# Performance work log

Measured on AMD Instinct MI355X. Metric: run time of the kernel, lower is better.

## Reference

```python
import jax, jax.numpy as jnp
import numpy as np


def _conv(x, w, pad):
    # NCHW conv, stride 1
    return jax.lax.conv_general_dilated(
        x, w, (1, 1), [(pad, pad), (pad, pad)],
        dimension_numbers=('NCHW', 'OIHW', 'NCHW'))


def _bn_relu(x, s, b, m, v):
    # eval-mode BatchNorm2d (running stats) + ReLU, eps=1e-5
    inv = s / jnp.sqrt(v + 1e-5)
    return jax.nn.relu(x * inv[None, :, None, None] + (b - m * inv)[None, :, None, None])


def _pam(x, qw, qb, kw, kb, vw, vb, gamma):
    B, C, H, W = x.shape
    N = H * W
    q = (_conv(x, qw, 0) + qb[None, :, None, None]).reshape(B, -1, N)  # [B,Cr,N]
    k = (_conv(x, kw, 0) + kb[None, :, None, None]).reshape(B, -1, N)  # [B,Cr,N]
    v = (_conv(x, vw, 0) + vb[None, :, None, None]).reshape(B, C, N)   # [B,C,N]
    energy = jnp.einsum('bcn,bcm->bnm', q, k)          # [B,N,N], query n over keys m
    att = jax.nn.softmax(energy, axis=-1)
    out = jnp.einsum('bcm,bnm->bcn', v, att).reshape(B, C, H, W)
    return gamma * out + x


def _cam(x, gamma):
    B, C, H, W = x.shape
    f = x.reshape(B, C, -1)                            # [B,C,N]
    energy = jnp.einsum('bcn,bdn->bcd', f, f)          # [B,C,C]
    energy_new = jnp.max(energy, axis=-1, keepdims=True) - energy
    att = jax.nn.softmax(energy_new, axis=-1)
    out = jnp.einsum('bcd,bdn->bcn', att, f).reshape(B, C, H, W)
    return gamma * out + x


def _forward(x, w5a, bn5a_s, bn5a_b, bn5a_m, bn5a_v,
             pq_w, pq_b, pk_w, pk_b, pv_w, pv_b, p_gamma,
             w51, bn51_s, bn51_b, bn51_m, bn51_v,
             w5c, bn5c_s, bn5c_b, bn5c_m, bn5c_v, c_gamma,
             w52, bn52_s, bn52_b, bn52_m, bn52_v,
             w8, b8):
    feat1 = _bn_relu(_conv(x, w5a, 1), bn5a_s, bn5a_b, bn5a_m, bn5a_v)
    sa_feat = _pam(feat1, pq_w, pq_b, pk_w, pk_b, pv_w, pv_b, p_gamma)
    sa_conv = _bn_relu(_conv(sa_feat, w51, 1), bn51_s, bn51_b, bn51_m, bn51_v)
    feat2 = _bn_relu(_conv(x, w5c, 1), bn5c_s, bn5c_b, bn5c_m, bn5c_v)
    sc_feat = _cam(feat2, c_gamma)
    sc_conv = _bn_relu(_conv(sc_feat, w52, 1), bn52_s, bn52_b, bn52_m, bn52_v)
    feat_sum = sa_conv + sc_conv
    # conv8 = Dropout2d (identity in eval) -> 1x1 conv -> ReLU
    sasc = jax.nn.relu(_conv(feat_sum, w8, 0) + b8[None, :, None, None])
    return sasc


def setup_inputs() -> dict:
    key = jax.random.key(0)
    ks = iter(jax.random.split(key, 48))
    def rn(shape, scale=0.1):
        return jax.random.normal(next(ks), shape, jnp.float32) * scale
    def bn_params(c):
        s = rn((c,), 0.2) + 1.0
        b = rn((c,), 0.1)
        m = rn((c,), 0.1)
        v = jnp.abs(rn((c,), 0.5)) + 0.5
        return s, b, m, v
    Cin, Ci, Cout = 512, 32, 2
    Cr = max(1, Ci // 8)  # = 4
    inp = {}
    inp['x'] = jax.random.normal(next(ks), (4, Cin, 64, 64), jnp.float32)
    inp['w5a'] = rn((Ci, Cin, 3, 3), 0.05)
    inp['bn5a_s'], inp['bn5a_b'], inp['bn5a_m'], inp['bn5a_v'] = bn_params(Ci)
    inp['pq_w'] = rn((Cr, Ci, 1, 1)); inp['pq_b'] = rn((Cr,), 0.01)
    inp['pk_w'] = rn((Cr, Ci, 1, 1)); inp['pk_b'] = rn((Cr,), 0.01)
    inp['pv_w'] = rn((Ci, Ci, 1, 1)); inp['pv_b'] = rn((Ci,), 0.01)
    inp['p_gamma'] = jnp.full((1,), 0.5, jnp.float32)
    inp['w51'] = rn((Ci, Ci, 3, 3))
    inp['bn51_s'], inp['bn51_b'], inp['bn51_m'], inp['bn51_v'] = bn_params(Ci)
    inp['w5c'] = rn((Ci, Cin, 3, 3), 0.05)
    inp['bn5c_s'], inp['bn5c_b'], inp['bn5c_m'], inp['bn5c_v'] = bn_params(Ci)
    inp['c_gamma'] = jnp.full((1,), 0.5, jnp.float32)
    inp['w52'] = rn((Ci, Ci, 3, 3))
    inp['bn52_s'], inp['bn52_b'], inp['bn52_m'], inp['bn52_v'] = bn_params(Ci)
    inp['w8'] = rn((Cout, Ci, 1, 1)); inp['b8'] = rn((Cout,), 0.01)
    return inp


def reference(x, w5a, bn5a_s, bn5a_b, bn5a_m, bn5a_v,
              pq_w, pq_b, pk_w, pk_b, pv_w, pv_b, p_gamma,
              w51, bn51_s, bn51_b, bn51_m, bn51_v,
              w5c, bn5c_s, bn5c_b, bn5c_m, bn5c_v, c_gamma,
              w52, bn52_s, bn52_b, bn52_m, bn52_v,
              w8, b8):
    return _forward(x, w5a, bn5a_s, bn5a_b, bn5a_m, bn5a_v,
                    pq_w, pq_b, pk_w, pk_b, pv_w, pv_b, p_gamma,
                    w51, bn51_s, bn51_b, bn51_m, bn51_v,
                    w5c, bn5c_s, bn5c_b, bn5c_m, bn5c_v, c_gamma,
                    w52, bn52_s, bn52_b, bn52_m, bn52_v,
                    w8, b8)
```

## Files before the change

kernel.cpp:

```cpp
#include <hip/hip_runtime.h>
#include <hip/hip_bf16.h>


typedef __attribute__((ext_vector_type(8))) short bf16x8;
typedef __attribute__((ext_vector_type(4))) float f32x4;

#define O_WPK   0
#define O_W51P  147456
#define O_W52P  152064
#define O_BNA   156672
#define O_W8    156928
#define O_PQW   157000
#define O_PKW   157132
#define O_PVW   157264
#define O_GAM   158320
#define O_Q     158400
#define O_K     223936
#define O_ENE   453312
#define O_F1T   985792
#define O_F2T   1510080
#define O_V     2034368
#define O_SAT   2558656
#define O_SCT   2837440
#define O_XT    461504
#define O_CP    4922048
#define O_PO    4922048
#define O_PS    3116224
#define O_PE2   9437184

__device__ __forceinline__ unsigned short f2b(float f){
  __hip_bfloat16 h = __float2bfloat16(f);
  return *(unsigned short*)&h;
}

__global__ __launch_bounds__(256) void k_prep_nhwc(
  const float* __restrict__ x,
  const float* w5a, const float* w5c,
  const float* w51, const float* w52,
  const float* s0,const float* b0,const float* m0,const float* v0,
  const float* s1,const float* b1,const float* m1,const float* v1,
  const float* s2,const float* b2,const float* m2,const float* v2,
  const float* s3,const float* b3,const float* m3,const float* v3,
  const float* w8,const float* b8,
  const float* pqw,const float* pqb,const float* pkw,const float* pkb,
  const float* pvw,const float* pvb,const float* pg,const float* cg,
  float* ws)
{
  int bx = blockIdx.x;
  int tid = threadIdx.x;
  __shared__ unsigned short t16[64][65];
  if (bx < 2048){
    int y = bx & 63, ct = (bx >> 6) & 7, b = bx >> 9;
    int r0 = tid >> 4, c0 = (tid & 15) * 4;
    const float* xb = x + ((size_t)(b*512 + ct*64))*4096 + y*64;
    #pragma unroll
    for (int i = 0; i < 4; ++i){
      int row = r0 + i*16;
      float4 v = *(const float4*)(xb + (size_t)row*4096 + c0);
      t16[row][c0+0] = f2b(v.x);
      t16[row][c0+1] = f2b(v.y);
      t16[row][c0+2] = f2b(v.z);
      t16[row][c0+3] = f2b(v.w);
    }
    __syncthreads();
    int pixl = tid >> 2, q = tid & 3;
    unsigned short vs[16];
    #pragma unroll
    for (int j = 0; j < 16; ++j) vs[j] = t16[q*16 + j][pixl];
    unsigned u[8];
    #pragma unroll
    for (int j = 0; j < 8; ++j) u[j] = (unsigned)vs[2*j] | ((unsigned)vs[2*j+1] << 16);
    unsigned short* xt = (unsigned short*)(ws + O_XT);
    int cbl = ct*2 + (q>>1);
    size_t off = (((size_t)(b*16 + cbl)*66 + (y+1))*66 + (pixl+1))*32 + (q&1)*16;
    *(uint4*)(xt + off)     = make_uint4(u[0],u[1],u[2],u[3]);
    *(uint4*)(xt + off + 8) = make_uint4(u[4],u[5],u[6],u[7]);
    return;
  }
  int pbx = bx - 2048;
  if (pbx < 1152){
    int id = pbx*256 + tid;
    int tap = id >> 15;
    int r = id & 32767;
    int cb = r >> 11;
    int r2 = r & 2047;
    int co = r2 >> 5, ci = r2 & 31;
    int cin = cb*32 + ci;
    float v = (co < 32) ? w5a[co*4608 + cin*9 + tap] : w5c[(co-32)*4608 + cin*9 + tap];
    ((unsigned short*)ws)[id] = f2b(v);
    return;
  }
  if (pbx < 1231){
    int id = (pbx-1152)*256 + tid;
    if (id >= 20076) return;
    if (id < 9216){ int tap=id>>10, co=(id>>5)&31, ci=id&31;
      ((unsigned short*)(ws + O_W51P))[id] = f2b(w51[co*288 + ci*9 + tap]); return; }
    id -= 9216;
    if (id < 9216){ int tap=id>>10, co=(id>>5)&31, ci=id&31;
      ((unsigned short*)(ws + O_W52P))[id] = f2b(w52[co*288 + ci*9 + tap]); return; }
    id -= 9216;
    if (id < 256){
      int conv = id>>6, ab = (id>>5)&1, c = id&31;
      const float *S,*Bb,*M,*V;
      if (conv==0){S=s0;Bb=b0;M=m0;V=v0;} else if (conv==1){S=s1;Bb=b1;M=m1;V=v1;}
      else if (conv==2){S=s2;Bb=b2;M=m2;V=v2;} else {S=s3;Bb=b3;M=m3;V=v3;}
      float A = S[c] * rsqrtf(V[c] + 1e-5f);
      ws[O_BNA + conv*64 + ab*32 + c] = ab ? (Bb[c] - M[c]*A) : A;
      return; }
    id -= 256;
    if (id < 64){ ws[O_W8+id] = w8[id]; return; } id -= 64;
    if (id < 2){ ws[O_W8+64+id] = b8[id]; return; } id -= 2;
    if (id < 128){ ws[O_PQW+id] = pqw[id]; return; } id -= 128;
    if (id < 4){ ws[O_PQW+128+id] = pqb[id]; return; } id -= 4;
    if (id < 128){ ws[O_PKW+id] = pkw[id]; return; } id -= 128;
    if (id < 4){ ws[O_PKW+128+id] = pkb[id]; return; } id -= 4;
    if (id < 1024){ ws[O_PVW+id] = pvw[id]; return; } id -= 1024;
    if (id < 32){ ws[O_PVW+1024+id] = pvb[id]; return; } id -= 32;
    ws[O_GAM+id] = id ? cg[0] : pg[0];
    return;
  }
  {
    int i = (pbx-1231)*256 + tid;
    if (i >= 66560) return;
    int part = i & 3; int j = i >> 2;
    int rp = j % 260; int bc = j / 260;
    int py, px;
    if (rp < 66){ py = 0; px = rp; }
    else if (rp < 132){ py = 65; px = rp - 66; }
    else if (rp < 196){ py = rp - 131; px = 0; }
    else { py = rp - 195; px = 65; }
    size_t off = (((size_t)bc*66 + py)*66 + px)*32 + part*8;
    *(uint4*)((unsigned short*)(ws + O_XT) + off) = make_uint4(0,0,0,0);
  }
}

__global__ __launch_bounds__(256) void k_conv_mfma(float* __restrict__ ws){
  int mb = blockIdx.x;
  int ks = blockIdx.y;
  int b = mb >> 6, y = mb & 63;
  __shared__ unsigned short Bs[198*40];
  int tid = threadIdx.x;
  int w = tid >> 6, l = tid & 63;
  f32x4 zero = {0.f,0.f,0.f,0.f};
  f32x4 acc[4] = {zero, zero, zero, zero};
  const unsigned short* wp = (const unsigned short*)ws;
  const unsigned short* xt = (const unsigned short*)(ws + O_XT);
  int arow = w*16 + (l & 15);
  int kq = (l >> 4)*8;
  int i0 = tid, i1 = tid + 256, i2 = tid + 512, i3 = tid + 768;
  const unsigned short* slab0 = xt + ((size_t)((b*16 + ks*4)*66 + y))*2112;
  uint4 r0 = *(const uint4*)(slab0 + i0*8);
  uint4 r1 = *(const uint4*)(slab0 + i1*8);
  uint4 r2 = *(const uint4*)(slab0 + i2*8);
  uint4 r3 = (tid < 24) ? *(const uint4*)(slab0 + i3*8) : make_uint4(0,0,0,0);
  for (int cb4 = 0; cb4 < 4; ++cb4){
    int cb = ks*4 + cb4;
    __syncthreads();
    *(uint4*)&Bs[(i0>>2)*40 + (i0&3)*8] = r0;
    *(uint4*)&Bs[(i1>>2)*40 + (i1&3)*8] = r1;
    *(uint4*)&Bs[(i2>>2)*40 + (i2&3)*8] = r2;
    if (tid < 24) *(uint4*)&Bs[(i3>>2)*40 + (i3&3)*8] = r3;
    __syncthreads();
    if (cb4 < 3){
      const unsigned short* slab = xt + ((size_t)((b*16 + cb + 1)*66 + y))*2112;
      r0 = *(const uint4*)(slab + i0*8);
      r1 = *(const uint4*)(slab + i1*8);
      r2 = *(const uint4*)(slab + i2*8);
      if (tid < 24) r3 = *(const uint4*)(slab + i3*8);
    }
    #pragma unroll
    for (int tap = 0; tap < 9; ++tap){
      int dy = tap/3, dx = tap - dy*3;
      bf16x8 af = *(const bf16x8*)(wp + (size_t)(tap*16 + cb)*2048 + arow*32 + kq);
      #pragma unroll
      for (int pt = 0; pt < 4; ++pt){
        int pix = pt*16 + (l&15) + dx;
        bf16x8 bv = *(const bf16x8*)&Bs[(dy*66 + pix)*40 + kq];
        acc[pt] = __builtin_amdgcn_mfma_f32_16x16x32_bf16(af, bv, acc[pt], 0, 0, 0);
      }
    }
  }
  float* cp = ws + O_CP + ((size_t)(ks*4 + b))*262144;
  int co0 = w*16 + (l>>4)*4;
  #pragma unroll
  for (int pt = 0; pt < 4; ++pt){
    int pix = y*64 + pt*16 + (l & 15);
    *(f32x4*)&cp[(size_t)pix*64 + co0] = acc[pt];
  }
}

__global__ __launch_bounds__(256) void k_feat(float* __restrict__ ws){
  int bx = blockIdx.x;
  int tid = threadIdx.x;
  __shared__ float Fl[32][68];
  __shared__ float wqs[4][32], wks[4][32], wvs[32][32];
  if (bx < 512){
    int b = bx >> 7, chunk = bx & 127;
    for (int i = tid; i < 1280; i += 256){
      if (i < 128)      ((float*)wqs)[i]     = ws[O_PQW + i];
      else if (i < 256) ((float*)wks)[i-128] = ws[O_PKW + (i-128)];
      else              ((float*)wvs)[i-256] = ws[O_PVW + (i-256)];
    }
    int pix = tid >> 3, cg = tid & 7;
    int pixg = (chunk << 5) + pix;
    const float* cpb = ws + O_CP + (size_t)b*262144 + (size_t)pixg*64 + cg*8;
    f32x4 sa_ = *(const f32x4*)(cpb);
    f32x4 sb_ = *(const f32x4*)(cpb + 4);
    {
      f32x4 t0 = *(const f32x4*)(cpb + 1048576);
      f32x4 t1 = *(const f32x4*)(cpb + 1048576 + 4);
      f32x4 t2 = *(const f32x4*)(cpb + 2097152);
      f32x4 t3 = *(const f32x4*)(cpb + 2097152 + 4);
      f32x4 t4 = *(const f32x4*)(cpb + 3145728);
      f32x4 t5 = *(const f32x4*)(cpb + 3145728 + 4);
      sa_ = (sa_ + t0) + (t2 + t4);
      sb_ = (sb_ + t1) + (t3 + t5);
    }
    int co0 = cg*8;
    int conv = co0 >> 5, cc0 = co0 & 31;
    float v8[8];
    #pragma unroll
    for (int j = 0; j < 8; ++j){
      int c = cc0 + j;
      float A = ws[O_BNA + conv*64 + c], Bb = ws[O_BNA + conv*64 + 32 + c];
      float s = (j < 4) ? sa_[j] : sb_[j-4];
      v8[j] = fmaxf(A*s + Bb, 0.f);
    }
    float* fdst = ws + (conv == 0 ? O_F1T : O_F2T) + ((size_t)(b*4096 + pixg))*32 + cc0;
    *(f32x4*)(fdst)     = (f32x4){v8[0],v8[1],v8[2],v8[3]};
    *(f32x4*)(fdst + 4) = (f32x4){v8[4],v8[5],v8[6],v8[7]};
    *(f32x4*)&Fl[pix][co0]     = (f32x4){v8[0],v8[1],v8[2],v8[3]};
    *(f32x4*)&Fl[pix][co0 + 4] = (f32x4){v8[4],v8[5],v8[6],v8[7]};
    __syncthreads();
    if (tid < 128){
      int part = tid >> 5, pixl = tid & 31;
      int n = (chunk << 5) + pixl;
      float fv[32];
      #pragma unroll
      for (int c = 0; c < 32; ++c) fv[c] = Fl[pixl][c];
      float q = ws[O_PQW+128+part], k = ws[O_PKW+128+part];
      #pragma unroll
      for (int c = 0; c < 32; ++c){ q += wqs[part][c]*fv[c]; k += wks[part][c]*fv[c]; }
      ws[O_Q + (((b<<2)+part)<<12) + n] = q;
      ws[O_K + (((b<<2)+part)<<12) + n] = k;
      unsigned short* vbp = (unsigned short*)(ws + O_V);
      #pragma unroll
      for (int j2 = 0; j2 < 8; ++j2){
        int c2 = part*8 + j2;
        float v = ws[O_PVW+1024+c2];
        #pragma unroll
        for (int c = 0; c < 32; ++c) v += wvs[c2][c]*fv[c];
        vbp[(((b<<5)+c2)<<12) + n] = f2b(v);
      }
    }
    {
      int ce = tid >> 3, d0 = (tid & 7) * 4;
      float a0=0.f, a1=0.f, a2=0.f, a3=0.f;
      #pragma unroll 8
      for (int n = 0; n < 32; ++n){
        float fc = Fl[n][32 + ce];
        float f0 = Fl[n][32 + d0], f1 = Fl[n][32 + d0 + 1];
        float f2 = Fl[n][32 + d0 + 2], f3 = Fl[n][32 + d0 + 3];
        a0 = fmaf(fc, f0, a0); a1 = fmaf(fc, f1, a1);
        a2 = fmaf(fc, f2, a2); a3 = fmaf(fc, f3, a3);
      }
      float* pe = ws + O_PE2 + ((size_t)(b*128 + chunk))*1024 + ce*32 + d0;
      *(f32x4*)pe = (f32x4){a0, a1, a2, a3};
    }
    return;
  }
  {
    int i = (bx-512)*256 + tid;
    if (i >= 8320) return;
    int part = i & 3; int j = i >> 2;
    int arr = j / 1040; int rem = j - arr*1040;
    int b = rem / 260; int rp = rem % 260;
    int py, px;
    if (rp < 66){ py = 0; px = rp; }
    else if (rp < 132){ py = 65; px = rp - 66; }
    else if (rp < 196){ py = rp - 131; px = 0; }
    else { py = rp - 195; px = 65; }
    size_t off = (((size_t)(b*66) + py)*66 + px)*32 + part*8;
    unsigned short* base = (unsigned short*)(ws + O_SAT + arr*278784);
    *(uint4*)(base + off) = make_uint4(0,0,0,0);
  }
}

__global__ __launch_bounds__(256, 6) void k_pam_flash(float* __restrict__ ws){
  int nt = blockIdx.x;
  int b  = blockIdx.y;
  int ms = blockIdx.z;
  __shared__ float Ks[2][4][4][32];
  __shared__ float Ss[4][32];
  __shared__ float Os[4][32][36];
  int tid = threadIdx.x;
  int w = tid >> 6, l = tid & 63;
  int nn = l & 15, g = l >> 4;
  int n0 = (nt<<5) + nn;
  const float LOG2E = 1.44269504f;
  const float BIAS  = -28.8539008f;
  float q0[4], q1[4];
  #pragma unroll
  for (int cr=0;cr<4;++cr){
    q0[cr] = ws[O_Q + (((b<<2)+cr)<<12) + n0] * LOG2E;
    q1[cr] = ws[O_Q + (((b<<2)+cr)<<12) + n0 + 16] * LOG2E;
  }
  int e0i = l*2, cr_s = e0i >> 5, mm_s = e0i & 31;
  int mbase = ms*1024 + w*256;
  const float* ksrc = ws + O_K + (((b<<2)+cr_s)<<12) + mbase + mm_s;
  const unsigned short* vb = (const unsigned short*)(ws + O_V);
  int mo = g*8;
  const unsigned short* vp0 = vb + (((b<<5) + nn)<<12) + mbase + mo;
  const unsigned short* vp1 = vb + (((b<<5) + 16 + nn)<<12) + mbase + mo;
  f32x4 zero = {0.f,0.f,0.f,0.f};
  f32x4 acc00 = zero, acc01 = zero, acc10 = zero, acc11 = zero;
  float lsum0 = 0.f, lsum1 = 0.f;
  bf16x8 a0A = *(const bf16x8*)(vp0);
  bf16x8 a1A = *(const bf16x8*)(vp1);
  float2 kreg = *(const float2*)(ksrc);
  *(float2*)&Ks[0][w][cr_s][mm_s] = kreg;
  bf16x8 a0B, a1B;
  for (int ch = 0; ch < 8; ++ch){
    int buf = ch & 1;
    if (ch < 7){
      int mn = (ch+1)*32;
      a0B = *(const bf16x8*)(vp0 + mn);
      a1B = *(const bf16x8*)(vp1 + mn);
      kreg = *(const float2*)(ksrc + mn);
    }
    float e0[8], e1[8];
    {
      float4 ka, kb;
      ka = *(const float4*)&Ks[buf][w][0][mo];
      kb = *(const float4*)&Ks[buf][w][0][mo+4];
      e0[0]=fmaf(q0[0],ka.x,BIAS); e0[1]=fmaf(q0[0],ka.y,BIAS); e0[2]=fmaf(q0[0],ka.z,BIAS); e0[3]=fmaf(q0[0],ka.w,BIAS);
      e0[4]=fmaf(q0[0],kb.x,BIAS); e0[5]=fmaf(q0[0],kb.y,BIAS); e0[6]=fmaf(q0[0],kb.z,BIAS); e0[7]=fmaf(q0[0],kb.w,BIAS);
      e1[0]=fmaf(q1[0],ka.x,BIAS); e1[1]=fmaf(q1[0],ka.y,BIAS); e1[2]=fmaf(q1[0],ka.z,BIAS); e1[3]=fmaf(q1[0],ka.w,BIAS);
      e1[4]=fmaf(q1[0],kb.x,BIAS); e1[5]=fmaf(q1[0],kb.y,BIAS); e1[6]=fmaf(q1[0],kb.z,BIAS); e1[7]=fmaf(q1[0],kb.w,BIAS);
#define KACC(CR) \
      ka = *(const float4*)&Ks[buf][w][CR][mo]; \
      kb = *(const float4*)&Ks[buf][w][CR][mo+4]; \
      e0[0]=fmaf(q0[CR],ka.x,e0[0]); e0[1]=fmaf(q0[CR],ka.y,e0[1]); e0[2]=fmaf(q0[CR],ka.z,e0[2]); e0[3]=fmaf(q0[CR],ka.w,e0[3]); \
      e0[4]=fmaf(q0[CR],kb.x,e0[4]); e0[5]=fmaf(q0[CR],kb.y,e0[5]); e0[6]=fmaf(q0[CR],kb.z,e0[6]); e0[7]=fmaf(q0[CR],kb.w,e0[7]); \
      e1[0]=fmaf(q1[CR],ka.x,e1[0]); e1[1]=fmaf(q1[CR],ka.y,e1[1]); e1[2]=fmaf(q1[CR],ka.z,e1[2]); e1[3]=fmaf(q1[CR],ka.w,e1[3]); \
      e1[4]=fmaf(q1[CR],kb.x,e1[4]); e1[5]=fmaf(q1[CR],kb.y,e1[5]); e1[6]=fmaf(q1[CR],kb.z,e1[6]); e1[7]=fmaf(q1[CR],kb.w,e1[7]);
      KACC(1)
      KACC(2)
      KACC(3)
#undef KACC
    }
    union { bf16x8 v; unsigned short u[8]; } pb0, pb1;
    #pragma unroll
    for (int j=0;j<8;j++){ float p = __builtin_amdgcn_exp2f(e0[j]); lsum0 += p; pb0.u[j] = f2b(p); }
    #pragma unroll
    for (int j=0;j<8;j++){ float p = __builtin_amdgcn_exp2f(e1[j]); lsum1 += p; pb1.u[j] = f2b(p); }
    acc00 = __builtin_amdgcn_mfma_f32_16x16x32_bf16(a0A, pb0.v, acc00, 0, 0, 0);
    acc01 = __builtin_amdgcn_mfma_f32_16x16x32_bf16(a1A, pb0.v, acc01, 0, 0, 0);
    acc10 = __builtin_amdgcn_mfma_f32_16x16x32_bf16(a0A, pb1.v, acc10, 0, 0, 0);
    acc11 = __builtin_amdgcn_mfma_f32_16x16x32_bf16(a1A, pb1.v, acc11, 0, 0, 0);
    if (ch < 7){
      int nb = buf ^ 1;
      *(float2*)&Ks[nb][w][cr_s][mm_s] = kreg;
      a0A = a0B; a1A = a1B;
    }
  }
  lsum0 += __shfl_xor(lsum0, 16); lsum0 += __shfl_xor(lsum0, 32);
  lsum1 += __shfl_xor(lsum1, 16); lsum1 += __shfl_xor(lsum1, 32);
// ... 102 lines not shown
  size_t base = ((size_t)((b*66 + y+1)*66 + xcol+1))*32 + c0;
  *(uint4*)(sct + base)     = make_uint4(u[0],u[1],u[2],u[3]);
  *(uint4*)(sct + base + 8) = make_uint4(u[4],u[5],u[6],u[7]);
}

__global__ __launch_bounds__(256) void k_final_mfma(float* __restrict__ ws, float* __restrict__ out){
  int y = blockIdx.x, b = blockIdx.y;
  __shared__ unsigned short Bs[2*3*66*40];
  __shared__ float ep[2][2][2][16];
  int tid = threadIdx.x;
  int w = tid >> 6, l = tid & 63;
  int g = l >> 4, col = l & 15;
  const unsigned short* sat = (const unsigned short*)(ws + O_SAT);
  const unsigned short* sct = (const unsigned short*)(ws + O_SCT);
  for (int i = tid; i < 1584; i += 256){
    int row = i >> 2, part = i & 3;
    int conv = row / 198; int rr = row - conv*198;
    int dy = rr / 66; int pix = rr - dy*66;
    const unsigned short* src = (conv ? sct : sat) + ((size_t)((b*66 + y + dy)*66 + pix))*32 + part*8;
    *(uint4*)&Bs[(size_t)row*40 + part*8] = *(const uint4*)src;
  }
  __syncthreads();
  int cohalf = w & 1, ptbase = (w >> 1) * 2;
  const unsigned short* wp[2] = { (const unsigned short*)(ws + O_W51P), (const unsigned short*)(ws + O_W52P) };
  f32x4 zero = {0.f,0.f,0.f,0.f};
  f32x4 acc[2][2] = {{zero,zero},{zero,zero}};
  for (int dy = 0; dy < 3; ++dy){
    for (int dx = 0; dx < 3; ++dx){
      int tap = dy*3 + dx;
      #pragma unroll
      for (int conv = 0; conv < 2; ++conv){
        bf16x8 af = *(const bf16x8*)(wp[conv] + tap*1024 + (cohalf*16 + col)*32 + g*8);
        #pragma unroll
        for (int pt = 0; pt < 2; ++pt){
          int pix = (ptbase + pt)*16 + col + dx;
          bf16x8 bv = *(const bf16x8*)&Bs[(size_t)((conv*3 + dy)*66 + pix)*40 + g*8];
          acc[conv][pt] = __builtin_amdgcn_mfma_f32_16x16x32_bf16(af, bv, acc[conv][pt], 0, 0, 0);
        }
      }
    }
  }
  float p0[2], p1[2];
  #pragma unroll
  for (int pt = 0; pt < 2; ++pt){
    float s0 = 0.f, s1 = 0.f;
    #pragma unroll
    for (int r = 0; r < 4; ++r){
      int co = cohalf*16 + g*4 + r;
      float A1 = ws[O_BNA + 2*64 + co], B1 = ws[O_BNA + 2*64 + 32 + co];
      float A2 = ws[O_BNA + 3*64 + co], B2 = ws[O_BNA + 3*64 + 32 + co];
      float fs = fmaxf(A1*acc[0][pt][r] + B1, 0.f) + fmaxf(A2*acc[1][pt][r] + B2, 0.f);
      s0 += ws[O_W8 + co]*fs;
      s1 += ws[O_W8 + 32 + co]*fs;
    }
    s0 += __shfl_xor(s0, 16); s0 += __shfl_xor(s0, 32);
    s1 += __shfl_xor(s1, 16); s1 += __shfl_xor(s1, 32);
    p0[pt] = s0; p1[pt] = s1;
  }
  if (cohalf == 0 && l < 16){
    #pragma unroll
    for (int pt = 0; pt < 2; ++pt){ ep[w>>1][pt][0][l] = p0[pt]; ep[w>>1][pt][1][l] = p1[pt]; }
  }
  __syncthreads();
  if (cohalf == 1 && l < 16){
    float b80 = ws[O_W8 + 64], b81 = ws[O_W8 + 65];
    #pragma unroll
    for (int pt = 0; pt < 2; ++pt){
      int pix = y*64 + (w>>1)*32 + pt*16 + l;
      float o0 = p0[pt] + ep[w>>1][pt][0][l] + b80;
      float o1 = p1[pt] + ep[w>>1][pt][1][l] + b81;
      out[((b*2+0)<<12) + pix] = fmaxf(o0, 0.f);
      out[((b*2+1)<<12) + pix] = fmaxf(o1, 0.f);
    }
  }
}

extern "C" void kernel_launch(void* const* d_in, const int* in_sizes, int n_in,
                              void* d_out, int out_size, void* d_ws, size_t ws_size,
                              hipStream_t stream) {
  const float* x    = (const float*)d_in[0];
  float* ws = (float*)d_ws;
  float* out = (float*)d_out;

  k_prep_nhwc<<<3539, 256, 0, stream>>>(
      x,
      (const float*)d_in[1], (const float*)d_in[18],
      (const float*)d_in[13], (const float*)d_in[24],
      (const float*)d_in[2],(const float*)d_in[3],(const float*)d_in[4],(const float*)d_in[5],
      (const float*)d_in[19],(const float*)d_in[20],(const float*)d_in[21],(const float*)d_in[22],
      (const float*)d_in[14],(const float*)d_in[15],(const float*)d_in[16],(const float*)d_in[17],
      (const float*)d_in[25],(const float*)d_in[26],(const float*)d_in[27],(const float*)d_in[28],
      (const float*)d_in[29],(const float*)d_in[30],
      (const float*)d_in[6],(const float*)d_in[7],(const float*)d_in[8],(const float*)d_in[9],
      (const float*)d_in[10],(const float*)d_in[11],(const float*)d_in[12],(const float*)d_in[23],
      ws);
  k_conv_mfma<<<dim3(256,4), 256, 0, stream>>>(ws);
  k_feat<<<545, 256, 0, stream>>>(ws);
  k_pam_flash<<<dim3(128,4,4), 256, 0, stream>>>(ws);
  k_finred<<<528, 256, 0, stream>>>(ws);
  k_cam_out<<<128, 256, 0, stream>>>(ws);
  k_final_mfma<<<dim3(64,4), 256, 0, stream>>>(ws, out);
}
```

Measured before the change: 95.26 us.

## Fuse 3x3 conv with BN/ReLU and QKV projection, dropping split-K partials

Merges the MFMA conv kernel and the feature/projection kernel into one kernel. Each block now computes a half-row of 32 pixels across all 16 channel blocks with double-buffered LDS, instead of split-K over 4 slices. This removes the fp32 partial-sum buffer round trip through global memory and one kernel launch. The SAT/SCT padding zeroing moves into the prep kernel, and the workspace offsets are relocated to fit. The cost is that the fused conv grid has 512 blocks, each doing 4x longer serial K loops, so there is less parallelism per block.

```diff
diff --git a/kernel.cpp b/kernel.cpp
--- a/kernel.cpp
+++ b/kernel.cpp
@@ -20,13 +20,12 @@
 #define O_F1T   985792
 #define O_F2T   1510080
 #define O_V     2034368
-#define O_SAT   2558656
-#define O_SCT   2837440
 #define O_XT    461504
-#define O_CP    4922048
 #define O_PO    4922048
 #define O_PS    3116224
 #define O_PE2   9437184
+#define O_SAT   9961472
+#define O_SCT   10240256
 
 __device__ __forceinline__ unsigned short f2b(float f){
   __hip_bfloat16 h = __float2bfloat16(f);
@@ -119,7 +118,7 @@
     ws[O_GAM+id] = id ? cg[0] : pg[0];
     return;
   }
-  {
+  if (pbx < 1491){
     int i = (pbx-1231)*256 + tid;
     if (i >= 66560) return;
     int part = i & 3; int j = i >> 2;
@@ -131,146 +130,10 @@
     else { py = rp - 195; px = 65; }
     size_t off = (((size_t)bc*66 + py)*66 + px)*32 + part*8;
     *(uint4*)((unsigned short*)(ws + O_XT) + off) = make_uint4(0,0,0,0);
-  }
-}
-
-__global__ __launch_bounds__(256) void k_conv_mfma(float* __restrict__ ws){
-  int mb = blockIdx.x;
-  int ks = blockIdx.y;
-  int b = mb >> 6, y = mb & 63;
-  __shared__ unsigned short Bs[198*40];
-  int tid = threadIdx.x;
-  int w = tid >> 6, l = tid & 63;
-  f32x4 zero = {0.f,0.f,0.f,0.f};
-  f32x4 acc[4] = {zero, zero, zero, zero};
-  const unsigned short* wp = (const unsigned short*)ws;
-  const unsigned short* xt = (const unsigned short*)(ws + O_XT);
-  int arow = w*16 + (l & 15);
-  int kq = (l >> 4)*8;
-  int i0 = tid, i1 = tid + 256, i2 = tid + 512, i3 = tid + 768;
-  const unsigned short* slab0 = xt + ((size_t)((b*16 + ks*4)*66 + y))*2112;
-  uint4 r0 = *(const uint4*)(slab0 + i0*8);
-  uint4 r1 = *(const uint4*)(slab0 + i1*8);
-  uint4 r2 = *(const uint4*)(slab0 + i2*8);
-  uint4 r3 = (tid < 24) ? *(const uint4*)(slab0 + i3*8) : make_uint4(0,0,0,0);
-  for (int cb4 = 0; cb4 < 4; ++cb4){
-    int cb = ks*4 + cb4;
-    __syncthreads();
-    *(uint4*)&Bs[(i0>>2)*40 + (i0&3)*8] = r0;
-    *(uint4*)&Bs[(i1>>2)*40 + (i1&3)*8] = r1;
-    *(uint4*)&Bs[(i2>>2)*40 + (i2&3)*8] = r2;
-    if (tid < 24) *(uint4*)&Bs[(i3>>2)*40 + (i3&3)*8] = r3;
-    __syncthreads();
-    if (cb4 < 3){
-      const unsigned short* slab = xt + ((size_t)((b*16 + cb + 1)*66 + y))*2112;
-      r0 = *(const uint4*)(slab + i0*8);
-      r1 = *(const uint4*)(slab + i1*8);
-      r2 = *(const uint4*)(slab + i2*8);
-      if (tid < 24) r3 = *(const uint4*)(slab + i3*8);
-    }
-    #pragma unroll
-    for (int tap = 0; tap < 9; ++tap){
-      int dy = tap/3, dx = tap - dy*3;
-      bf16x8 af = *(const bf16x8*)(wp + (size_t)(tap*16 + cb)*2048 + arow*32 + kq);
-      #pragma unroll
-      for (int pt = 0; pt < 4; ++pt){
-        int pix = pt*16 + (l&15) + dx;
-        bf16x8 bv = *(const bf16x8*)&Bs[(dy*66 + pix)*40 + kq];
-        acc[pt] = __builtin_amdgcn_mfma_f32_16x16x32_bf16(af, bv, acc[pt], 0, 0, 0);
-      }
-    }
-  }
-  float* cp = ws + O_CP + ((size_t)(ks*4 + b))*262144;
-  int co0 = w*16 + (l>>4)*4;
-  #pragma unroll
-  for (int pt = 0; pt < 4; ++pt){
-    int pix = y*64 + pt*16 + (l & 15);
-    *(f32x4*)&cp[(size_t)pix*64 + co0] = acc[pt];
-  }
-}
-
-__global__ __launch_bounds__(256) void k_feat(float* __restrict__ ws){
-  int bx = blockIdx.x;
-  int tid = threadIdx.x;
-  __shared__ float Fl[32][68];
-  __shared__ float wqs[4][32], wks[4][32], wvs[32][32];
-  if (bx < 512){
-    int b = bx >> 7, chunk = bx & 127;
-    for (int i = tid; i < 1280; i += 256){
-      if (i < 128)      ((float*)wqs)[i]     = ws[O_PQW + i];
-      else if (i < 256) ((float*)wks)[i-128] = ws[O_PKW + (i-128)];
-      else              ((float*)wvs)[i-256] = ws[O_PVW + (i-256)];
-    }
-    int pix = tid >> 3, cg = tid & 7;
-    int pixg = (chunk << 5) + pix;
-    const float* cpb = ws + O_CP + (size_t)b*262144 + (size_t)pixg*64 + cg*8;
-    f32x4 sa_ = *(const f32x4*)(cpb);
-    f32x4 sb_ = *(const f32x4*)(cpb + 4);
-    {
-      f32x4 t0 = *(const f32x4*)(cpb + 1048576);
-      f32x4 t1 = *(const f32x4*)(cpb + 1048576 + 4);
-      f32x4 t2 = *(const f32x4*)(cpb + 2097152);
-      f32x4 t3 = *(const f32x4*)(cpb + 2097152 + 4);
-      f32x4 t4 = *(const f32x4*)(cpb + 3145728);
-      f32x4 t5 = *(const f32x4*)(cpb + 3145728 + 4);
-      sa_ = (sa_ + t0) + (t2 + t4);
-      sb_ = (sb_ + t1) + (t3 + t5);
-    }
-    int co0 = cg*8;
-    int conv = co0 >> 5, cc0 = co0 & 31;
-    float v8[8];
-    #pragma unroll
-    for (int j = 0; j < 8; ++j){
-      int c = cc0 + j;
-      float A = ws[O_BNA + conv*64 + c], Bb = ws[O_BNA + conv*64 + 32 + c];
-      float s = (j < 4) ? sa_[j] : sb_[j-4];
-      v8[j] = fmaxf(A*s + Bb, 0.f);
-    }
-    float* fdst = ws + (conv == 0 ? O_F1T : O_F2T) + ((size_t)(b*4096 + pixg))*32 + cc0;
-    *(f32x4*)(fdst)     = (f32x4){v8[0],v8[1],v8[2],v8[3]};
-    *(f32x4*)(fdst + 4) = (f32x4){v8[4],v8[5],v8[6],v8[7]};
-    *(f32x4*)&Fl[pix][co0]     = (f32x4){v8[0],v8[1],v8[2],v8[3]};
-    *(f32x4*)&Fl[pix][co0 + 4] = (f32x4){v8[4],v8[5],v8[6],v8[7]};
-    __syncthreads();
-    if (tid < 128){
-      int part = tid >> 5, pixl = tid & 31;
-      int n = (chunk << 5) + pixl;
-      float fv[32];
-      #pragma unroll
-      for (int c = 0; c < 32; ++c) fv[c] = Fl[pixl][c];
-      float q = ws[O_PQW+128+part], k = ws[O_PKW+128+part];
-      #pragma unroll
-      for (int c = 0; c < 32; ++c){ q += wqs[part][c]*fv[c]; k += wks[part][c]*fv[c]; }
-      ws[O_Q + (((b<<2)+part)<<12) + n] = q;
-      ws[O_K + (((b<<2)+part)<<12) + n] = k;
-      unsigned short* vbp = (unsigned short*)(ws + O_V);
-      #pragma unroll
-      for (int j2 = 0; j2 < 8; ++j2){
-        int c2 = part*8 + j2;
-        float v = ws[O_PVW+1024+c2];
-        #pragma unroll
-        for (int c = 0; c < 32; ++c) v += wvs[c2][c]*fv[c];
-        vbp[(((b<<5)+c2)<<12) + n] = f2b(v);
-      }
-    }
-    {
-      int ce = tid >> 3, d0 = (tid & 7) * 4;
-      float a0=0.f, a1=0.f, a2=0.f, a3=0.f;
-      #pragma unroll 8
-      for (int n = 0; n < 32; ++n){
-        float fc = Fl[n][32 + ce];
-        float f0 = Fl[n][32 + d0], f1 = Fl[n][32 + d0 + 1];
-        float f2 = Fl[n][32 + d0 + 2], f3 = Fl[n][32 + d0 + 3];
-        a0 = fmaf(fc, f0, a0); a1 = fmaf(fc, f1, a1);
-        a2 = fmaf(fc, f2, a2); a3 = fmaf(fc, f3, a3);
-      }
-      float* pe = ws + O_PE2 + ((size_t)(b*128 + chunk))*1024 + ce*32 + d0;
-      *(f32x4*)pe = (f32x4){a0, a1, a2, a3};
-    }
     return;
   }
   {
-    int i = (bx-512)*256 + tid;
+    int i = (pbx-1491)*256 + tid;
     if (i >= 8320) return;
     int part = i & 3; int j = i >> 2;
     int arr = j / 1040; int rem = j - arr*1040;
@@ -281,8 +144,138 @@
     else if (rp < 196){ py = rp - 131; px = 0; }
     else { py = rp - 195; px = 65; }
     size_t off = (((size_t)(b*66) + py)*66 + px)*32 + part*8;
-    unsigned short* base = (unsigned short*)(ws + O_SAT + arr*278784);
+    unsigned short* base = (unsigned short*)(ws + (arr ? O_SCT : O_SAT));
     *(uint4*)(base + off) = make_uint4(0,0,0,0);
+  }
+}
+
+__global__ __launch_bounds__(256) void k_convfeat(float* __restrict__ ws){
+  int bx = blockIdx.x;
+  int b  = blockIdx.y;
+  int y = bx >> 1, xh = bx & 1;
+  __shared__ unsigned short Bs[2][102*40];
+  __shared__ float Fl[32][68];
+  __shared__ float wqs[4][32], wks[4][32], wvs[32][32];
+  int tid = threadIdx.x;
+  int w = tid >> 6, l = tid & 63;
+  for (int i = tid; i < 1280; i += 256){
+    if (i < 128)      ((float*)wqs)[i]     = ws[O_PQW + i];
+    else if (i < 256) ((float*)wks)[i-128] = ws[O_PKW + (i-128)];
+    else              ((float*)wvs)[i-256] = ws[O_PVW + (i-256)];
+  }
+  const unsigned short* wp = (const unsigned short*)ws;
+  const unsigned short* xt = (const unsigned short*)(ws + O_XT);
+  int arow = w*16 + (l & 15);
+  int kq = (l >> 4)*8;
+  int dyA = tid/136, remA = tid - dyA*136;
+  int t1 = tid + 256;
+  int dyB = t1/136, remB = t1 - dyB*136;
+  int c0o = dyA*2112 + xh*1024 + remA*8;
+  int c1o = dyB*2112 + xh*1024 + remB*8;
+  int s0o = (dyA*34 + (remA>>2))*40 + (remA&3)*8;
+  int s1o = (dyB*34 + (remB>>2))*40 + (remB&3)*8;
+  bool hasB = (tid < 152);
+  f32x4 zero = {0.f,0.f,0.f,0.f};
+  f32x4 acc0 = zero, acc1 = zero;
+  uint4 rA0, rA1, rB0, rB1;
+
+#define CF_LOAD(R0, R1, CB) { \
+    const unsigned short* pb_ = xt + ((size_t)((b*16+(CB))*66 + y))*2112; \
+    R0 = *(const uint4*)(pb_ + c0o); \
+    if (hasB) R1 = *(const uint4*)(pb_ + c1o); }
+
+#define CF_WRITE(BUF, R0, R1) { \
+    *(uint4*)&Bs[BUF][s0o] = R0; \
+    if (hasB) *(uint4*)&Bs[BUF][s1o] = R1; }
+
+#define CF_COMPUTE(BUF, CB) { \
+    _Pragma("unroll") \
+    for (int tap = 0; tap < 9; ++tap){ \
+      int dy = tap/3, dx = tap - dy*3; \
+      bf16x8 af = *(const bf16x8*)(wp + (size_t)(tap*16 + (CB))*2048 + arow*32 + kq); \
+      bf16x8 bv0 = *(const bf16x8*)&Bs[BUF][(dy*34 + (l&15) + dx)*40 + kq]; \
+      bf16x8 bv1 = *(const bf16x8*)&Bs[BUF][(dy*34 + 16 + (l&15) + dx)*40 + kq]; \
+      acc0 = __builtin_amdgcn_mfma_f32_16x16x32_bf16(af, bv0, acc0, 0, 0, 0); \
+      acc1 = __builtin_amdgcn_mfma_f32_16x16x32_bf16(af, bv1, acc1, 0, 0, 0); \
+    } }
+
+  CF_LOAD(rA0, rA1, 0)
+  CF_LOAD(rB0, rB1, 1)
+  #pragma unroll 1
+  for (int cb2 = 0; cb2 < 8; ++cb2){
+    int cbA = cb2*2;
+    __syncthreads();
+    CF_WRITE(0, rA0, rA1)
+    __syncthreads();
+    if (cb2 < 7) CF_LOAD(rA0, rA1, cbA + 2)
+    CF_COMPUTE(0, cbA)
+    __syncthreads();
+    CF_WRITE(1, rB0, rB1)
+    __syncthreads();
+    if (cb2 < 7) CF_LOAD(rB0, rB1, cbA + 3)
+    CF_COMPUTE(1, cbA + 1)
+  }
+#undef CF_LOAD
+#undef CF_WRITE
+#undef CF_COMPUTE
+
+  {
+    int co0 = w*16 + (l>>4)*4;
+    int conv = co0 >> 5;
+    #pragma unroll
+    for (int r = 0; r < 4; ++r){
+      int c = (co0 + r) & 31;
+      float A = ws[O_BNA + conv*64 + c], Bb = ws[O_BNA + conv*64 + 32 + c];
+      Fl[l & 15][co0 + r]        = fmaxf(A*acc0[r] + Bb, 0.f);
+      Fl[16 + (l & 15)][co0 + r] = fmaxf(A*acc1[r] + Bb, 0.f);
+    }
+  }
+  __syncthreads();
+  int chunk = bx;
+  {
+    int pix = tid >> 3, cg = tid & 7;
+    int pixg = (chunk << 5) + pix;
+    int co0 = cg*8, conv = co0 >> 5, cc0 = co0 & 31;
+    f32x4 v0 = *(const f32x4*)&Fl[pix][co0];
+    f32x4 v1 = *(const f32x4*)&Fl[pix][co0 + 4];
+    float* fdst = ws + (conv == 0 ? O_F1T : O_F2T) + ((size_t)(b*4096 + pixg))*32 + cc0;
+    *(f32x4*)(fdst)     = v0;
+    *(f32x4*)(fdst + 4) = v1;
+  }
+  if (tid < 128){
+    int part = tid >> 5, pixl = tid & 31;
+    int n = (chunk << 5) + pixl;
+    float fv[32];
+    #pragma unroll
+    for (int c = 0; c < 32; ++c) fv[c] = Fl[pixl][c];
+    float q = ws[O_PQW+128+part], k = ws[O_PKW+128+part];
+    #pragma unroll
+    for (int c = 0; c < 32; ++c){ q += wqs[part][c]*fv[c]; k += wks[part][c]*fv[c]; }
+    ws[O_Q + (((b<<2)+part)<<12) + n] = q;
+    ws[O_K + (((b<<2)+part)<<12) + n] = k;
+    unsigned short* vbp = (unsigned short*)(ws + O_V);
+    #pragma unroll
+    for (int j2 = 0; j2 < 8; ++j2){
+      int c2 = part*8 + j2;
+      float v = ws[O_PVW+1024+c2];
+      #pragma unroll
+      for (int c = 0; c < 32; ++c) v += wvs[c2][c]*fv[c];
+      vbp[(((b<<5)+c2)<<12) + n] = f2b(v);
+    }
+  }
+  {
+    int ce = tid >> 3, d0 = (tid & 7) * 4;
+    float a0=0.f, a1=0.f, a2=0.f, a3=0.f;
+    #pragma unroll 8
+    for (int n = 0; n < 32; ++n){
+      float fc = Fl[n][32 + ce];
+      float f0 = Fl[n][32 + d0], f1 = Fl[n][32 + d0 + 1];
+      float f2 = Fl[n][32 + d0 + 2], f3 = Fl[n][32 + d0 + 3];
+      a0 = fmaf(fc, f0, a0); a1 = fmaf(fc, f1, a1);
+      a2 = fmaf(fc, f2, a2); a3 = fmaf(fc, f3, a3);
+    }
+    float* pe = ws + O_PE2 + ((size_t)(b*128 + chunk))*1024 + ce*32 + d0;
+    *(f32x4*)pe = (f32x4){a0, a1, a2, a3};
   }
 }
 
@@ -551,7 +544,7 @@
   float* ws = (float*)d_ws;
   float* out = (float*)d_out;
 
-  k_prep_nhwc<<<3539, 256, 0, stream>>>(
+  k_prep_nhwc<<<3572, 256, 0, stream>>>(
       x,
       (const float*)d_in[1], (const float*)d_in[18],
       (const float*)d_in[13], (const float*)d_in[24],
@@ -563,8 +556,7 @@
       (const float*)d_in[6],(const float*)d_in[7],(const float*)d_in[8],(const float*)d_in[9],
       (const float*)d_in[10],(const float*)d_in[11],(const float*)d_in[12],(const float*)d_in[23],
       ws);
-  k_conv_mfma<<<dim3(256,4), 256, 0, stream>>>(ws);
-  k_feat<<<545, 256, 0, stream>>>(ws);
+  k_convfeat<<<dim3(128,4), 256, 0, stream>>>(ws);
   k_pam_flash<<<dim3(128,4,4), 256, 0, stream>>>(ws);
   k_finred<<<528, 256, 0, stream>>>(ws);
   k_cam_out<<<128, 256, 0, stream>>>(ws);
```

Measured after the change: 96.87 us. About the same (+1.7%).

## Split conv row tiles in half and move SAT/SCT border zeroing into prep

Applied to the files above, without the earlier changes.

The 3x3 conv MFMA kernel now gives each block half an output row (32 pixels) instead of a full row, which doubles the grid to 2048 blocks and shrinks the shared-memory slab. The aim is more parallelism and occupancy for the conv stage. The cost is that each half-row block reloads its overlapping input halo and the weight fragments. Zeroing of the padded SAT/SCT border buffers moves from k_feat into k_prep_nhwc, with SAT/SCT relocated to a non-overlapping workspace region, so k_feat no longer carries extra tail blocks.

```diff
diff --git a/kernel.cpp b/kernel.cpp
--- a/kernel.cpp
+++ b/kernel.cpp
@@ -20,13 +20,13 @@
 #define O_F1T   985792
 #define O_F2T   1510080
 #define O_V     2034368
-#define O_SAT   2558656
-#define O_SCT   2837440
 #define O_XT    461504
 #define O_CP    4922048
 #define O_PO    4922048
 #define O_PS    3116224
 #define O_PE2   9437184
+#define O_SAT   9961472
+#define O_SCT   10240256
 
 __device__ __forceinline__ unsigned short f2b(float f){
   __hip_bfloat16 h = __float2bfloat16(f);
@@ -119,7 +119,7 @@
     ws[O_GAM+id] = id ? cg[0] : pg[0];
     return;
   }
-  {
+  if (pbx < 1491){
     int i = (pbx-1231)*256 + tid;
     if (i >= 66560) return;
     int part = i & 3; int j = i >> 2;
@@ -131,146 +131,10 @@
     else { py = rp - 195; px = 65; }
     size_t off = (((size_t)bc*66 + py)*66 + px)*32 + part*8;
     *(uint4*)((unsigned short*)(ws + O_XT) + off) = make_uint4(0,0,0,0);
-  }
-}
-
-__global__ __launch_bounds__(256) void k_conv_mfma(float* __restrict__ ws){
-  int mb = blockIdx.x;
-  int ks = blockIdx.y;
-  int b = mb >> 6, y = mb & 63;
-  __shared__ unsigned short Bs[198*40];
-  int tid = threadIdx.x;
-  int w = tid >> 6, l = tid & 63;
-  f32x4 zero = {0.f,0.f,0.f,0.f};
-  f32x4 acc[4] = {zero, zero, zero, zero};
-  const unsigned short* wp = (const unsigned short*)ws;
-  const unsigned short* xt = (const unsigned short*)(ws + O_XT);
-  int arow = w*16 + (l & 15);
-  int kq = (l >> 4)*8;
-  int i0 = tid, i1 = tid + 256, i2 = tid + 512, i3 = tid + 768;
-  const unsigned short* slab0 = xt + ((size_t)((b*16 + ks*4)*66 + y))*2112;
-  uint4 r0 = *(const uint4*)(slab0 + i0*8);
-  uint4 r1 = *(const uint4*)(slab0 + i1*8);
-  uint4 r2 = *(const uint4*)(slab0 + i2*8);
-  uint4 r3 = (tid < 24) ? *(const uint4*)(slab0 + i3*8) : make_uint4(0,0,0,0);
-  for (int cb4 = 0; cb4 < 4; ++cb4){
-    int cb = ks*4 + cb4;
-    __syncthreads();
-    *(uint4*)&Bs[(i0>>2)*40 + (i0&3)*8] = r0;
-    *(uint4*)&Bs[(i1>>2)*40 + (i1&3)*8] = r1;
-    *(uint4*)&Bs[(i2>>2)*40 + (i2&3)*8] = r2;
-    if (tid < 24) *(uint4*)&Bs[(i3>>2)*40 + (i3&3)*8] = r3;
-    __syncthreads();
-    if (cb4 < 3){
-      const unsigned short* slab = xt + ((size_t)((b*16 + cb + 1)*66 + y))*2112;
-      r0 = *(const uint4*)(slab + i0*8);
-      r1 = *(const uint4*)(slab + i1*8);
-      r2 = *(const uint4*)(slab + i2*8);
-      if (tid < 24) r3 = *(const uint4*)(slab + i3*8);
-    }
-    #pragma unroll
-    for (int tap = 0; tap < 9; ++tap){
-      int dy = tap/3, dx = tap - dy*3;
-      bf16x8 af = *(const bf16x8*)(wp + (size_t)(tap*16 + cb)*2048 + arow*32 + kq);
-      #pragma unroll
-      for (int pt = 0; pt < 4; ++pt){
-        int pix = pt*16 + (l&15) + dx;
-        bf16x8 bv = *(const bf16x8*)&Bs[(dy*66 + pix)*40 + kq];
-        acc[pt] = __builtin_amdgcn_mfma_f32_16x16x32_bf16(af, bv, acc[pt], 0, 0, 0);
-      }
-    }
-  }
-  float* cp = ws + O_CP + ((size_t)(ks*4 + b))*262144;
-  int co0 = w*16 + (l>>4)*4;
-  #pragma unroll
-  for (int pt = 0; pt < 4; ++pt){
-    int pix = y*64 + pt*16 + (l & 15);
-    *(f32x4*)&cp[(size_t)pix*64 + co0] = acc[pt];
-  }
-}
-
-__global__ __launch_bounds__(256) void k_feat(float* __restrict__ ws){
-  int bx = blockIdx.x;
-  int tid = threadIdx.x;
-  __shared__ float Fl[32][68];
-  __shared__ float wqs[4][32], wks[4][32], wvs[32][32];
-  if (bx < 512){
-    int b = bx >> 7, chunk = bx & 127;
-    for (int i = tid; i < 1280; i += 256){
-      if (i < 128)      ((float*)wqs)[i]     = ws[O_PQW + i];
-      else if (i < 256) ((float*)wks)[i-128] = ws[O_PKW + (i-128)];
-      else              ((float*)wvs)[i-256] = ws[O_PVW + (i-256)];
-    }
-    int pix = tid >> 3, cg = tid & 7;
-    int pixg = (chunk << 5) + pix;
-    const float* cpb = ws + O_CP + (size_t)b*262144 + (size_t)pixg*64 + cg*8;
-    f32x4 sa_ = *(const f32x4*)(cpb);
-    f32x4 sb_ = *(const f32x4*)(cpb + 4);
-    {
-      f32x4 t0 = *(const f32x4*)(cpb + 1048576);
-      f32x4 t1 = *(const f32x4*)(cpb + 1048576 + 4);
-      f32x4 t2 = *(const f32x4*)(cpb + 2097152);
-      f32x4 t3 = *(const f32x4*)(cpb + 2097152 + 4);
-      f32x4 t4 = *(const f32x4*)(cpb + 3145728);
-      f32x4 t5 = *(const f32x4*)(cpb + 3145728 + 4);
-      sa_ = (sa_ + t0) + (t2 + t4);
-      sb_ = (sb_ + t1) + (t3 + t5);
-    }
-    int co0 = cg*8;
-    int conv = co0 >> 5, cc0 = co0 & 31;
-    float v8[8];
-    #pragma unroll
-    for (int j = 0; j < 8; ++j){
-      int c = cc0 + j;
-      float A = ws[O_BNA + conv*64 + c], Bb = ws[O_BNA + conv*64 + 32 + c];
-      float s = (j < 4) ? sa_[j] : sb_[j-4];
-      v8[j] = fmaxf(A*s + Bb, 0.f);
-    }
-    float* fdst = ws + (conv == 0 ? O_F1T : O_F2T) + ((size_t)(b*4096 + pixg))*32 + cc0;
-    *(f32x4*)(fdst)     = (f32x4){v8[0],v8[1],v8[2],v8[3]};
-    *(f32x4*)(fdst + 4) = (f32x4){v8[4],v8[5],v8[6],v8[7]};
-    *(f32x4*)&Fl[pix][co0]     = (f32x4){v8[0],v8[1],v8[2],v8[3]};
-    *(f32x4*)&Fl[pix][co0 + 4] = (f32x4){v8[4],v8[5],v8[6],v8[7]};
-    __syncthreads();
-    if (tid < 128){
-      int part = tid >> 5, pixl = tid & 31;
-      int n = (chunk << 5) + pixl;
-      float fv[32];
-      #pragma unroll
-      for (int c = 0; c < 32; ++c) fv[c] = Fl[pixl][c];
-      float q = ws[O_PQW+128+part], k = ws[O_PKW+128+part];
-      #pragma unroll
-      for (int c = 0; c < 32; ++c){ q += wqs[part][c]*fv[c]; k += wks[part][c]*fv[c]; }
-      ws[O_Q + (((b<<2)+part)<<12) + n] = q;
-      ws[O_K + (((b<<2)+part)<<12) + n] = k;
-      unsigned short* vbp = (unsigned short*)(ws + O_V);
-      #pragma unroll
-      for (int j2 = 0; j2 < 8; ++j2){
-        int c2 = part*8 + j2;
-        float v = ws[O_PVW+1024+c2];
-        #pragma unroll
-        for (int c = 0; c < 32; ++c) v += wvs[c2][c]*fv[c];
-        vbp[(((b<<5)+c2)<<12) + n] = f2b(v);
-      }
-    }
-    {
-      int ce = tid >> 3, d0 = (tid & 7) * 4;
-      float a0=0.f, a1=0.f, a2=0.f, a3=0.f;
-      #pragma unroll 8
-      for (int n = 0; n < 32; ++n){
-        float fc = Fl[n][32 + ce];
-        float f0 = Fl[n][32 + d0], f1 = Fl[n][32 + d0 + 1];
-        float f2 = Fl[n][32 + d0 + 2], f3 = Fl[n][32 + d0 + 3];
-        a0 = fmaf(fc, f0, a0); a1 = fmaf(fc, f1, a1);
-        a2 = fmaf(fc, f2, a2); a3 = fmaf(fc, f3, a3);
-      }
-      float* pe = ws + O_PE2 + ((size_t)(b*128 + chunk))*1024 + ce*32 + d0;
-      *(f32x4*)pe = (f32x4){a0, a1, a2, a3};
-    }
     return;
   }
   {
-    int i = (bx-512)*256 + tid;
+    int i = (pbx-1491)*256 + tid;
     if (i >= 8320) return;
     int part = i & 3; int j = i >> 2;
     int arr = j / 1040; int rem = j - arr*1040;
@@ -281,8 +145,145 @@
     else if (rp < 196){ py = rp - 131; px = 0; }
     else { py = rp - 195; px = 65; }
     size_t off = (((size_t)(b*66) + py)*66 + px)*32 + part*8;
-    unsigned short* base = (unsigned short*)(ws + O_SAT + arr*278784);
+    unsigned short* base = (unsigned short*)(ws + (arr ? O_SCT : O_SAT));
     *(uint4*)(base + off) = make_uint4(0,0,0,0);
+  }
+}
+
+__global__ __launch_bounds__(256) void k_conv_mfma(float* __restrict__ ws){
+  int mb = blockIdx.x;
+  int ks = blockIdx.y;
+  int b = mb >> 7;
+  int y = (mb >> 1) & 63;
+  int xh = mb & 1;
+  __shared__ unsigned short Bs[102*40];
+  int tid = threadIdx.x;
+  int w = tid >> 6, l = tid & 63;
+  f32x4 zero = {0.f,0.f,0.f,0.f};
+  f32x4 acc0 = zero, acc1 = zero;
+  const unsigned short* wp = (const unsigned short*)ws;
+  const unsigned short* xt = (const unsigned short*)(ws + O_XT);
+  int arow = w*16 + (l & 15);
+  int kq = (l >> 4)*8;
+  int dyA = tid/136, remA = tid - dyA*136;
+  int t1 = tid + 256;
+  int dyB = t1/136, remB = t1 - dyB*136;
+  int c0o = dyA*2112 + xh*1024 + remA*8;
+  int c1o = dyB*2112 + xh*1024 + remB*8;
+  int s0o = (dyA*34 + (remA>>2))*40 + (remA&3)*8;
+  int s1o = (dyB*34 + (remB>>2))*40 + (remB&3)*8;
+  bool hasB = (tid < 152);
+  uint4 rA0, rA1;
+  {
+    const unsigned short* pb_ = xt + ((size_t)((b*16 + ks*4)*66 + y))*2112;
+    rA0 = *(const uint4*)(pb_ + c0o);
+    if (hasB) rA1 = *(const uint4*)(pb_ + c1o);
+  }
+  #pragma unroll 1
+  for (int cb4 = 0; cb4 < 4; ++cb4){
+    int cb = ks*4 + cb4;
+    __syncthreads();
+    *(uint4*)&Bs[s0o] = rA0;
+    if (hasB) *(uint4*)&Bs[s1o] = rA1;
+    __syncthreads();
+    if (cb4 < 3){
+      const unsigned short* pb_ = xt + ((size_t)((b*16 + cb + 1)*66 + y))*2112;
+      rA0 = *(const uint4*)(pb_ + c0o);
+      if (hasB) rA1 = *(const uint4*)(pb_ + c1o);
+    }
+    #pragma unroll
+    for (int tap = 0; tap < 9; ++tap){
+      int dy = tap/3, dx = tap - dy*3;
+      bf16x8 af = *(const bf16x8*)(wp + (size_t)(tap*16 + cb)*2048 + arow*32 + kq);
+      bf16x8 bv0 = *(const bf16x8*)&Bs[(dy*34 + (l&15) + dx)*40 + kq];
+      bf16x8 bv1 = *(const bf16x8*)&Bs[(dy*34 + 16 + (l&15) + dx)*40 + kq];
+      acc0 = __builtin_amdgcn_mfma_f32_16x16x32_bf16(af, bv0, acc0, 0, 0, 0);
+      acc1 = __builtin_amdgcn_mfma_f32_16x16x32_bf16(af, bv1, acc1, 0, 0, 0);
+    }
+  }
+  float* cp = ws + O_CP + ((size_t)(ks*4 + b))*262144;
+  int co0 = w*16 + (l>>4)*4;
+  int pixb = y*64 + xh*32 + (l & 15);
+  *(f32x4*)&cp[(size_t)pixb*64 + co0]        = acc0;
+  *(f32x4*)&cp[(size_t)(pixb+16)*64 + co0]   = acc1;
+}
+
+__global__ __launch_bounds__(256) void k_feat(float* __restrict__ ws){
+  int bx = blockIdx.x;
+  int tid = threadIdx.x;
+  __shared__ float Fl[32][68];
+  __shared__ float wqs[4][32], wks[4][32], wvs[32][32];
+  int b = bx >> 7, chunk = bx & 127;
+  for (int i = tid; i < 1280; i += 256){
+    if (i < 128)      ((float*)wqs)[i]     = ws[O_PQW + i];
+    else if (i < 256) ((float*)wks)[i-128] = ws[O_PKW + (i-128)];
+    else              ((float*)wvs)[i-256] = ws[O_PVW + (i-256)];
+  }
+  int pix = tid >> 3, cg = tid & 7;
+  int pixg = (chunk << 5) + pix;
+  const float* cpb = ws + O_CP + (size_t)b*262144 + (size_t)pixg*64 + cg*8;
+  f32x4 sa_ = *(const f32x4*)(cpb);
+  f32x4 sb_ = *(const f32x4*)(cpb + 4);
+  {
+    f32x4 t0 = *(const f32x4*)(cpb + 1048576);
+    f32x4 t1 = *(const f32x4*)(cpb + 1048576 + 4);
+    f32x4 t2 = *(const f32x4*)(cpb + 2097152);
+    f32x4 t3 = *(const f32x4*)(cpb + 2097152 + 4);
+    f32x4 t4 = *(const f32x4*)(cpb + 3145728);
+    f32x4 t5 = *(const f32x4*)(cpb + 3145728 + 4);
+    sa_ = (sa_ + t0) + (t2 + t4);
+    sb_ = (sb_ + t1) + (t3 + t5);
+  }
+  int co0 = cg*8;
+  int conv = co0 >> 5, cc0 = co0 & 31;
+  float v8[8];
+  #pragma unroll
+  for (int j = 0; j < 8; ++j){
+    int c = cc0 + j;
+    float A = ws[O_BNA + conv*64 + c], Bb = ws[O_BNA + conv*64 + 32 + c];
+    float s = (j < 4) ? sa_[j] : sb_[j-4];
+    v8[j] = fmaxf(A*s + Bb, 0.f);
+  }
+  float* fdst = ws + (conv == 0 ? O_F1T : O_F2T) + ((size_t)(b*4096 + pixg))*32 + cc0;
+  *(f32x4*)(fdst)     = (f32x4){v8[0],v8[1],v8[2],v8[3]};
+  *(f32x4*)(fdst + 4) = (f32x4){v8[4],v8[5],v8[6],v8[7]};
+  *(f32x4*)&Fl[pix][co0]     = (f32x4){v8[0],v8[1],v8[2],v8[3]};
+  *(f32x4*)&Fl[pix][co0 + 4] = (f32x4){v8[4],v8[5],v8[6],v8[7]};
+  __syncthreads();
+  if (tid < 128){
+    int part = tid >> 5, pixl = tid & 31;
+    int n = (chunk << 5) + pixl;
+    float fv[32];
+    #pragma unroll
+    for (int c = 0; c < 32; ++c) fv[c] = Fl[pixl][c];
+    float q = ws[O_PQW+128+part], k = ws[O_PKW+128+part];
+    #pragma unroll
+    for (int c = 0; c < 32; ++c){ q += wqs[part][c]*fv[c]; k += wks[part][c]*fv[c]; }
+    ws[O_Q + (((b<<2)+part)<<12) + n] = q;
+    ws[O_K + (((b<<2)+part)<<12) + n] = k;
+    unsigned short* vbp = (unsigned short*)(ws + O_V);
+    #pragma unroll
+    for (int j2 = 0; j2 < 8; ++j2){
+      int c2 = part*8 + j2;
+      float v = ws[O_PVW+1024+c2];
+      #pragma unroll
+      for (int c = 0; c < 32; ++c) v += wvs[c2][c]*fv[c];
+      vbp[(((b<<5)+c2)<<12) + n] = f2b(v);
+    }
+  }
+  {
+    int ce = tid >> 3, d0 = (tid & 7) * 4;
+    float a0=0.f, a1=0.f, a2=0.f, a3=0.f;
+    #pragma unroll 8
+    for (int n = 0; n < 32; ++n){
+      float fc = Fl[n][32 + ce];
+      float f0 = Fl[n][32 + d0], f1 = Fl[n][32 + d0 + 1];
+      float f2 = Fl[n][32 + d0 + 2], f3 = Fl[n][32 + d0 + 3];
+      a0 = fmaf(fc, f0, a0); a1 = fmaf(fc, f1, a1);
+      a2 = fmaf(fc, f2, a2); a3 = fmaf(fc, f3, a3);
+    }
+    float* pe = ws + O_PE2 + ((size_t)(b*128 + chunk))*1024 + ce*32 + d0;
+    *(f32x4*)pe = (f32x4){a0, a1, a2, a3};
   }
 }
 
@@ -551,7 +552,7 @@
   float* ws = (float*)d_ws;
   float* out = (float*)d_out;
 
-  k_prep_nhwc<<<3539, 256, 0, stream>>>(
+  k_prep_nhwc<<<3572, 256, 0, stream>>>(
       x,
       (const float*)d_in[1], (const float*)d_in[18],
       (const float*)d_in[13], (const float*)d_in[24],
@@ -563,8 +564,8 @@
       (const float*)d_in[6],(const float*)d_in[7],(const float*)d_in[8],(const float*)d_in[9],
       (const float*)d_in[10],(const float*)d_in[11],(const float*)d_in[12],(const float*)d_in[23],
       ws);
-  k_conv_mfma<<<dim3(256,4), 256, 0, stream>>>(ws);
-  k_feat<<<545, 256, 0, stream>>>(ws);
+  k_conv_mfma<<<dim3(512,4), 256, 0, stream>>>(ws);
+  k_feat<<<512, 256, 0, stream>>>(ws);
   k_pam_flash<<<dim3(128,4,4), 256, 0, stream>>>(ws);
   k_finred<<<528, 256, 0, stream>>>(ws);
   k_cam_out<<<128, 256, 0, stream>>>(ws);
```

Result: slower. 101.5 us (+6.6%).
